# Kernel tuning notes

Hardware: AMD Instinct MI355X
Metric: run time of the kernel (lower is better)

The kernel has to match this reference:

```python
import jax, jax.numpy as jnp
import numpy as np

SIGMA_PRIOR = 0.5   # sigma init kwarg; logvar_prior = log(sigma), sigma_prior = exp(logvar_prior) = sigma
TEMP = 1.0
LN_EPS = 1e-5
DIM, NQ, NK = 256, 512, 512


def setup_inputs() -> dict:
    key = jax.random.key(0)
    ks = jax.random.split(key, 10)
    s = 1.0 / np.sqrt(DIM)
    return {
        "Q": jax.random.normal(ks[0], (NQ, DIM), jnp.float32),
        "K": jax.random.normal(ks[1], (NK, DIM), jnp.float32),
        "V": jax.random.normal(ks[2], (NK, DIM), jnp.float32),
        "eps": jax.random.normal(ks[3], (NQ, NK), jnp.float32),
        # prior MLP: Linear(dim,dim) -> ReLU -> Linear(dim,1)
        "W1p": jax.random.normal(ks[4], (DIM, DIM), jnp.float32) * s,
        "b1p": jnp.zeros((DIM,), jnp.float32),
        "w2p": jax.random.normal(ks[5], (DIM,), jnp.float32) * s,
        "b2p": jnp.zeros((), jnp.float32),
        # posterior MLP: Linear(2*dim, dim) -> ReLU
        "Wpost": jax.random.normal(ks[6], (DIM, 2 * DIM), jnp.float32) * s,
        "bpost": jnp.zeros((DIM,), jnp.float32),
        # mu / logvar heads: Linear(dim, 1)
        "w_mu": jax.random.normal(ks[7], (DIM,), jnp.float32) * s,
        "b_mu": jnp.zeros((), jnp.float32),
        "w_lv": jax.random.normal(ks[8], (DIM,), jnp.float32) * s,
        "b_lv": jnp.zeros((), jnp.float32),
        # output LayerNorm(dim)
        "gamma": jnp.ones((DIM,), jnp.float32),
        "beta": jnp.zeros((DIM,), jnp.float32),
    }


def reference(Q, K, V, eps, W1p, b1p, w2p, b2p, Wpost, bpost,
              w_mu, b_mu, w_lv, b_lv, gamma, beta):
    dim = Q.shape[-1]
    sigma_prior = jnp.float32(SIGMA_PRIOR)

    # --- prior: mlp_prior(K) per key; broadcast over queries (identical math to K_exp) ---
    h = jax.nn.relu(K @ W1p.T + b1p)                       # [Nk, dim]
    mu_prior = h @ w2p + b2p - 0.5 * sigma_prior ** 2      # [Nk]

    # --- posterior: Linear on cat([Q_exp, K_exp]) == Q@Wq^T + K@Wk^T + b ---
    Wq, Wk = Wpost[:, :dim], Wpost[:, dim:]
    latent = jax.nn.relu((Q @ Wq.T)[:, None, :] + (K @ Wk.T + bpost)[None, :, :])  # [Nq, Nk, dim]
    phi = latent @ w_mu + b_mu                             # [Nq, Nk]
    logvar = latent @ w_lv + b_lv                          # [Nq, Nk]
    sig = jnp.exp(0.5 * logvar)
    mu = phi - 0.5 * sig ** 2

    # --- KL(prior || posterior form used by the module) ---
    term0 = jnp.log(sigma_prior / sig)
    term1 = (sig ** 2 + (mu - mu_prior[None, :]) ** 2) / (2.0 * sigma_prior ** 2)
    kl = jnp.mean(term0 + term1 - 0.5)

    # --- reparameterized sample, softmax weights, context ---
    samples = jnp.exp(mu + sig * eps) / TEMP               # [Nq, Nk]
    weights = jax.nn.softmax(samples, axis=-1)
    context = weights @ V                                  # [Nq, dim]

    # --- LayerNorm(dim) ---
    m = jnp.mean(context, axis=-1, keepdims=True)
    v = jnp.var(context, axis=-1, keepdims=True)
    out = (context - m) / jnp.sqrt(v + LN_EPS) * gamma + beta
    return (out, kl)
```

## Files before the change

kernel.cpp:

```cpp
#include <hip/hip_runtime.h>
#include <math.h>

#define DIM 256
#define NQ  512
#define NK  512

#define WS_A   0
#define WS_B   (NQ*DIM)
#define WS_MP  (WS_B + NK*DIM)
#define WS_S   (WS_MP + 512)
#define WS_P   (WS_S + NQ*NK)

__global__ __launch_bounds__(512) void k1_precompute(
    const float* __restrict__ Q, const float* __restrict__ Km,
    const float* __restrict__ W1p, const float* __restrict__ b1p,
    const float* __restrict__ w2p, const float* __restrict__ b2p,
    const float* __restrict__ Wpost, const float* __restrict__ bpost,
    float* __restrict__ A, float* __restrict__ B, float* __restrict__ mu_prior)
{
    __shared__ float X_lds[4][DIM];
    __shared__ float red[2][4][260];
    const int tid = threadIdx.x;
    const int bid = blockIdx.x;

    const int job = bid >> 7;
    const int r0  = (bid & 127) * 4;
    const float* X = (job == 0) ? Q : Km;
    const float* W = (job == 2) ? W1p : Wpost;
    const int wstride = (job == 2) ? DIM : 2 * DIM;
    const int wcol    = (job == 1) ? DIM : 0;

    if (tid < 256) {
        int row = tid >> 6, c4 = tid & 63;
        *(float4*)&X_lds[row][c4 * 4] = *(const float4*)&X[(r0 + row) * DIM + c4 * 4];
    }
    __syncthreads();

    const int c  = tid & 255;
    const int dh = tid >> 8;
    const float* wrow = W + c * wstride + wcol + dh * 128;
    const float* xrow0 = &X_lds[0][dh * 128];

    float acc0 = 0.f, acc1 = 0.f, acc2 = 0.f, acc3 = 0.f;
    #pragma unroll 8
    for (int d0 = 0; d0 < 128; d0 += 4) {
        float4 w4 = *(const float4*)&wrow[d0];
        float4 x0 = *(const float4*)&xrow0[d0];
        float4 x1 = *(const float4*)&xrow0[DIM + d0];
        float4 x2 = *(const float4*)&xrow0[2 * DIM + d0];
        float4 x3 = *(const float4*)&xrow0[3 * DIM + d0];
        acc0 = fmaf(x0.x, w4.x, acc0); acc0 = fmaf(x0.y, w4.y, acc0);
        acc0 = fmaf(x0.z, w4.z, acc0); acc0 = fmaf(x0.w, w4.w, acc0);
        acc1 = fmaf(x1.x, w4.x, acc1); acc1 = fmaf(x1.y, w4.y, acc1);
        acc1 = fmaf(x1.z, w4.z, acc1); acc1 = fmaf(x1.w, w4.w, acc1);
        acc2 = fmaf(x2.x, w4.x, acc2); acc2 = fmaf(x2.y, w4.y, acc2);
        acc2 = fmaf(x2.z, w4.z, acc2); acc2 = fmaf(x2.w, w4.w, acc2);
        acc3 = fmaf(x3.x, w4.x, acc3); acc3 = fmaf(x3.y, w4.y, acc3);
        acc3 = fmaf(x3.z, w4.z, acc3); acc3 = fmaf(x3.w, w4.w, acc3);
    }
    red[dh][0][c] = acc0; red[dh][1][c] = acc1;
    red[dh][2][c] = acc2; red[dh][3][c] = acc3;
    __syncthreads();

    if (job < 2) {
        if (tid < 256) {
            #pragma unroll
            for (int r = 0; r < 4; ++r) {
                float v = red[0][r][c] + red[1][r][c];
                if (job == 0) A[(r0 + r) * DIM + c] = v;
                else          B[(r0 + r) * DIM + c] = v + bpost[c];
            }
        }
    } else {
        if (tid < 256) {
            float b1 = b1p[c], w2 = w2p[c];
            #pragma unroll
            for (int r = 0; r < 4; ++r)
                red[0][r][c] = fmaxf(red[0][r][c] + red[1][r][c] + b1, 0.f) * w2;
        }
        __syncthreads();
        int w = tid >> 6, lane = tid & 63;
        if (w < 4) {
            float v = red[0][w][lane] + red[0][w][lane + 64]
                    + red[0][w][lane + 128] + red[0][w][lane + 192];
            #pragma unroll
            for (int off = 32; off; off >>= 1) v += __shfl_xor(v, off);
            if (lane == 0) mu_prior[r0 + w] = v + b2p[0] - 0.125f;
        }
    }
}

__global__ __launch_bounds__(512) void k2_latent(
    const float* __restrict__ A, const float* __restrict__ B,
    const float* __restrict__ mu_prior, const float* __restrict__ eps,
    const float* __restrict__ w_mu, const float* __restrict__ b_mu,
    const float* __restrict__ w_lv, const float* __restrict__ b_lv,
    float* __restrict__ samples, float* __restrict__ partials)
{
    __shared__ float A_lds[32][260];
    __shared__ float B_lds[32][260];
    __shared__ float wm[DIM], wl[DIM];
    __shared__ float red[2][256][9];
    __shared__ float wred[8];
    const int tid = threadIdx.x;
    const int bq0 = (blockIdx.x >> 4) * 32;
    const int bk0 = (blockIdx.x & 15) * 32;

    #pragma unroll
    for (int i = 0; i < 4; ++i) {
        int f4 = tid + 512 * i;
        int row = f4 >> 6, c4 = f4 & 63;
        *(float4*)&A_lds[row][c4 * 4] = *(const float4*)&A[(bq0 + row) * DIM + c4 * 4];
        *(float4*)&B_lds[row][c4 * 4] = *(const float4*)&B[(bk0 + row) * DIM + c4 * 4];
    }
    if (tid < 256) { wm[tid] = w_mu[tid]; wl[tid] = w_lv[tid]; }
    __syncthreads();

    const int l  = tid & 255;
    const int dh = tid >> 8;
    const int tq = l >> 4, tk = l & 15;
    const int db = dh * 128;

    float p00 = 0, p01 = 0, p10 = 0, p11 = 0;
    float l00 = 0, l01 = 0, l10 = 0, l11 = 0;

    #pragma unroll 4
    for (int dd = 0; dd < 128; dd += 4) {
        int d0 = db + dd;
        float4 a0 = *(const float4*)&A_lds[tq][d0];
        float4 a1 = *(const float4*)&A_lds[tq + 16][d0];
        float4 b0 = *(const float4*)&B_lds[tk][d0];
        float4 b1 = *(const float4*)&B_lds[tk + 16][d0];
        float4 m4 = *(const float4*)&wm[d0];
        float4 v4 = *(const float4*)&wl[d0];
#define STEP(c) { float r_;                                                      \
        r_ = fmaxf(a0.c + b0.c, 0.f); p00 = fmaf(r_, m4.c, p00); l00 = fmaf(r_, v4.c, l00); \
        r_ = fmaxf(a0.c + b1.c, 0.f); p01 = fmaf(r_, m4.c, p01); l01 = fmaf(r_, v4.c, l01); \
        r_ = fmaxf(a1.c + b0.c, 0.f); p10 = fmaf(r_, m4.c, p10); l10 = fmaf(r_, v4.c, l10); \
        r_ = fmaxf(a1.c + b1.c, 0.f); p11 = fmaf(r_, m4.c, p11); l11 = fmaf(r_, v4.c, l11); }
        STEP(x) STEP(y) STEP(z) STEP(w)
#undef STEP
    }

    red[dh][l][0] = p00; red[dh][l][1] = l00;
    red[dh][l][2] = p01; red[dh][l][3] = l01;
    red[dh][l][4] = p10; red[dh][l][5] = l10;
    red[dh][l][6] = p11; red[dh][l][7] = l11;
    __syncthreads();

    float kls = 0.f;
    if (tid < 256) {
        const float bmu = b_mu[0], blv = b_lv[0];
        const int qa = bq0 + tq, qb = qa + 16;
        const int ka = bk0 + tk, kb = ka + 16;
        const float mpa = mu_prior[ka], mpb = mu_prior[kb];
        const float C0 = -0.69314718056f - 0.5f;

#define FINISH(i, q, k, mp) {                                        \
        float pacc = red[0][tid][2*(i)]   + red[1][tid][2*(i)];      \
        float lacc = red[0][tid][2*(i)+1] + red[1][tid][2*(i)+1];    \
        float lv   = lacc + blv;                                     \
        float phi  = pacc + bmu;                                     \
        float sig  = __expf(0.5f * lv);                              \
        float sig2 = sig * sig;                                      \
        float mu   = phi - 0.5f * sig2;                              \
        float dm   = mu - (mp);                                      \
        kls += C0 - 0.5f * lv + 2.f * (sig2 + dm * dm);              \
        samples[(q) * NK + (k)] = __expf(mu + sig * eps[(q) * NK + (k)]); }

        FINISH(0, qa, ka, mpa)
        FINISH(1, qa, kb, mpb)
        FINISH(2, qb, ka, mpa)
        FINISH(3, qb, kb, mpb)
#undef FINISH
    }

    #pragma unroll
    for (int off = 32; off; off >>= 1) kls += __shfl_xor(kls, off);
    if ((tid & 63) == 0) wred[tid >> 6] = kls;
    __syncthreads();
    if (tid == 0) {
        float s = 0.f;
        #pragma unroll
        for (int i = 0; i < 8; ++i) s += wred[i];
        partials[blockIdx.x] = s;
    }
}

__global__ __launch_bounds__(512) void k3_output(
    const float* __restrict__ samples, const float* __restrict__ V,
    const float* __restrict__ gamma, const float* __restrict__ beta,
    const float* __restrict__ partials, float* __restrict__ out)
{
    __shared__ float w_lds[2][NK];
    __shared__ float redbuf[16][DIM];
    __shared__ float sred[8], sred2[8], klr[8], sinv[2];
    const int tid = threadIdx.x;
    const int q0 = blockIdx.x * 2;

    if (blockIdx.x == 0) {
        float v = (tid < 256) ? partials[tid] : 0.f;
        #pragma unroll
        for (int off = 32; off; off >>= 1) v += __shfl_xor(v, off);
        if ((tid & 63) == 0) klr[tid >> 6] = v;
        __syncthreads();
        if (tid == 0) {
            float s = 0.f;
            #pragma unroll
            for (int i = 0; i < 8; ++i) s += klr[i];
            out[NQ * DIM] = s * (1.f / (float)(NQ * NK));
        }
    }

    #pragma unroll
    for (int r = 0; r < 2; ++r) {
        float sv = samples[(q0 + r) * NK + tid];
        float m = sv;
        #pragma unroll
        for (int off = 32; off; off >>= 1) m = fmaxf(m, __shfl_xor(m, off));
        if ((tid & 63) == 0) sred[tid >> 6] = m;
        __syncthreads();
        m = fmaxf(fmaxf(fmaxf(sred[0], sred[1]), fmaxf(sred[2], sred[3])),
                  fmaxf(fmaxf(sred[4], sred[5]), fmaxf(sred[6], sred[7])));
        float e = __expf(sv - m);
        w_lds[r][tid] = e;
        float sum = e;
        #pragma unroll
        for (int off = 32; off; off >>= 1) sum += __shfl_xor(sum, off);
        __syncthreads();
        if ((tid & 63) == 0) sred[tid >> 6] = sum;
        __syncthreads();
        if (tid == 0) {
            float s = 0.f;
            #pragma unroll
            for (int i = 0; i < 8; ++i) s += sred[i];
            sinv[r] = 1.f / s;
        }
        __syncthreads();
    }

    const int g = tid & 63, s = tid >> 6;
    float a00 = 0, a01 = 0, a02 = 0, a03 = 0;
    float a10 = 0, a11 = 0, a12 = 0, a13 = 0;
    const float* vp = V + s * 64 * DIM + 4 * g;
    #pragma unroll 8
    for (int i = 0; i < 64; ++i) {
        float4 v4 = *(const float4*)(vp + i * DIM);
        int k = s * 64 + i;
        float w0 = w_lds[0][k], w1 = w_lds[1][k];
        a00 = fmaf(w0, v4.x, a00); a01 = fmaf(w0, v4.y, a01);
        a02 = fmaf(w0, v4.z, a02); a03 = fmaf(w0, v4.w, a03);
        a10 = fmaf(w1, v4.x, a10); a11 = fmaf(w1, v4.y, a11);
        a12 = fmaf(w1, v4.z, a12); a13 = fmaf(w1, v4.w, a13);
    }
    *(float4*)&redbuf[s * 2 + 0][4 * g] = make_float4(a00, a01, a02, a03);
    *(float4*)&redbuf[s * 2 + 1][4 * g] = make_float4(a10, a11, a12, a13);
    __syncthreads();

    const int r = tid >> 8, col = tid & 255;
    float c = 0.f;
    #pragma unroll
    for (int j = 0; j < 8; ++j) c += redbuf[j * 2 + r][col];
    c *= sinv[r];
    float s1v = c, s2v = c * c;
    #pragma unroll
    for (int off = 32; off; off >>= 1) {
        s1v += __shfl_xor(s1v, off);
        s2v += __shfl_xor(s2v, off);
    }
    if ((tid & 63) == 0) { sred[tid >> 6] = s1v; sred2[tid >> 6] = s2v; }
    __syncthreads();
    float mean = (sred[4 * r] + sred[4 * r + 1] + sred[4 * r + 2] + sred[4 * r + 3]) * (1.f / DIM);
    float msq  = (sred2[4 * r] + sred2[4 * r + 1] + sred2[4 * r + 2] + sred2[4 * r + 3]) * (1.f / DIM);
    float var  = msq - mean * mean;
    out[(q0 + r) * DIM + col] = (c - mean) * rsqrtf(var + 1e-5f) * gamma[col] + beta[col];
}

extern "C" void kernel_launch(void* const* d_in, const int* in_sizes, int n_in,
                              void* d_out, int out_size, void* d_ws, size_t ws_size,
                              hipStream_t stream)
{
    (void)in_sizes; (void)n_in; (void)out_size; (void)ws_size;
    const float* Q     = (const float*)d_in[0];
    const float* K     = (const float*)d_in[1];
    const float* V     = (const float*)d_in[2];
    const float* eps   = (const float*)d_in[3];
    const float* W1p   = (const float*)d_in[4];
    const float* b1p   = (const float*)d_in[5];
    const float* w2p   = (const float*)d_in[6];
    const float* b2p   = (const float*)d_in[7];
    const float* Wpost = (const float*)d_in[8];
    const float* bpost = (const float*)d_in[9];
    const float* w_mu  = (const float*)d_in[10];
    const float* b_mu  = (const float*)d_in[11];
    const float* w_lv  = (const float*)d_in[12];
    const float* b_lv  = (const float*)d_in[13];
    const float* gamma = (const float*)d_in[14];
    const float* beta  = (const float*)d_in[15];
    float* out = (float*)d_out;
    float* wsf = (float*)d_ws;

    float* A        = wsf + WS_A;
    float* B        = wsf + WS_B;
    float* mu_prior = wsf + WS_MP;
    float* samples  = wsf + WS_S;
    float* partials = wsf + WS_P;

    k1_precompute<<<dim3(384), dim3(512), 0, stream>>>(
        Q, K, W1p, b1p, w2p, b2p, Wpost, bpost, A, B, mu_prior);
    k2_latent<<<dim3(256), dim3(512), 0, stream>>>(
        A, B, mu_prior, eps, w_mu, b_mu, w_lv, b_lv, samples, partials);
    k3_output<<<dim3(256), dim3(512), 0, stream>>>(
        samples, V, gamma, beta, partials, out);
}
```

Before: 123.2 us.

## Fuse three kernels into one cooperative kernel with grid-wide syncs

Replaces the three separate launches (precompute, latent, output) with a single cooperative kernel of 256 blocks that uses grid.sync() between phases and a union of shared-memory layouts. To fit the phase-1 work into 256 blocks, the Q/K projection blocks now process 8 rows each instead of 4. The aim is to remove the launch gaps and inter-kernel drain between stages. In exchange it adds grid-barrier cost, and the first phase has fewer, heavier blocks.

Result: slower. 196.9 us (+59.8%).

```diff
diff --git a/kernel.cpp b/kernel.cpp
--- a/kernel.cpp
+++ b/kernel.cpp
@@ -1,5 +1,8 @@
 #include <hip/hip_runtime.h>
+#include <hip/hip_cooperative_groups.h>
 #include <math.h>
+
+namespace cg = cooperative_groups;
 
 #define DIM 256
 #define NQ  512
@@ -11,269 +14,293 @@
 #define WS_S   (WS_MP + 512)
 #define WS_P   (WS_S + NQ*NK)
 
-__global__ __launch_bounds__(512) void k1_precompute(
+struct P1 {
+    float X[8][DIM];
+    float red[2][8][260];
+};
+struct P2 {
+    float A[32][260];
+    float B[32][260];
+    float wm[DIM], wl[DIM];
+    float red[2][256][9];
+    float wred[8];
+};
+struct P3 {
+    float w[2][NK];
+    float redbuf[16][DIM];
+    float sred[8], sred2[8], klr[8], sinv[2];
+};
+union SmemU { P1 p1; P2 p2; P3 p3; };
+
+__global__ __launch_bounds__(512) void fused_kernel(
     const float* __restrict__ Q, const float* __restrict__ Km,
+    const float* __restrict__ V, const float* __restrict__ eps,
     const float* __restrict__ W1p, const float* __restrict__ b1p,
     const float* __restrict__ w2p, const float* __restrict__ b2p,
     const float* __restrict__ Wpost, const float* __restrict__ bpost,
-    float* __restrict__ A, float* __restrict__ B, float* __restrict__ mu_prior)
-{
-    __shared__ float X_lds[4][DIM];
-    __shared__ float red[2][4][260];
-    const int tid = threadIdx.x;
-    const int bid = blockIdx.x;
-
-    const int job = bid >> 7;
-    const int r0  = (bid & 127) * 4;
-    const float* X = (job == 0) ? Q : Km;
-    const float* W = (job == 2) ? W1p : Wpost;
-    const int wstride = (job == 2) ? DIM : 2 * DIM;
-    const int wcol    = (job == 1) ? DIM : 0;
-
-    if (tid < 256) {
-        int row = tid >> 6, c4 = tid & 63;
-        *(float4*)&X_lds[row][c4 * 4] = *(const float4*)&X[(r0 + row) * DIM + c4 * 4];
-    }
-    __syncthreads();
-
-    const int c  = tid & 255;
-    const int dh = tid >> 8;
-    const float* wrow = W + c * wstride + wcol + dh * 128;
-    const float* xrow0 = &X_lds[0][dh * 128];
-
-    float acc0 = 0.f, acc1 = 0.f, acc2 = 0.f, acc3 = 0.f;
-    #pragma unroll 8
-    for (int d0 = 0; d0 < 128; d0 += 4) {
-        float4 w4 = *(const float4*)&wrow[d0];
-        float4 x0 = *(const float4*)&xrow0[d0];
-        float4 x1 = *(const float4*)&xrow0[DIM + d0];
-        float4 x2 = *(const float4*)&xrow0[2 * DIM + d0];
-        float4 x3 = *(const float4*)&xrow0[3 * DIM + d0];
-        acc0 = fmaf(x0.x, w4.x, acc0); acc0 = fmaf(x0.y, w4.y, acc0);
-        acc0 = fmaf(x0.z, w4.z, acc0); acc0 = fmaf(x0.w, w4.w, acc0);
-        acc1 = fmaf(x1.x, w4.x, acc1); acc1 = fmaf(x1.y, w4.y, acc1);
-        acc1 = fmaf(x1.z, w4.z, acc1); acc1 = fmaf(x1.w, w4.w, acc1);
-        acc2 = fmaf(x2.x, w4.x, acc2); acc2 = fmaf(x2.y, w4.y, acc2);
-        acc2 = fmaf(x2.z, w4.z, acc2); acc2 = fmaf(x2.w, w4.w, acc2);
-        acc3 = fmaf(x3.x, w4.x, acc3); acc3 = fmaf(x3.y, w4.y, acc3);
-        acc3 = fmaf(x3.z, w4.z, acc3); acc3 = fmaf(x3.w, w4.w, acc3);
-    }
-    red[dh][0][c] = acc0; red[dh][1][c] = acc1;
-    red[dh][2][c] = acc2; red[dh][3][c] = acc3;
-    __syncthreads();
-
-    if (job < 2) {
-        if (tid < 256) {
-            #pragma unroll
-            for (int r = 0; r < 4; ++r) {
-                float v = red[0][r][c] + red[1][r][c];
-                if (job == 0) A[(r0 + r) * DIM + c] = v;
-                else          B[(r0 + r) * DIM + c] = v + bpost[c];
-            }
-        }
-    } else {
-        if (tid < 256) {
-            float b1 = b1p[c], w2 = w2p[c];
-            #pragma unroll
-            for (int r = 0; r < 4; ++r)
-                red[0][r][c] = fmaxf(red[0][r][c] + red[1][r][c] + b1, 0.f) * w2;
-        }
-        __syncthreads();
-        int w = tid >> 6, lane = tid & 63;
-        if (w < 4) {
-            float v = red[0][w][lane] + red[0][w][lane + 64]
-                    + red[0][w][lane + 128] + red[0][w][lane + 192];
-            #pragma unroll
-            for (int off = 32; off; off >>= 1) v += __shfl_xor(v, off);
-            if (lane == 0) mu_prior[r0 + w] = v + b2p[0] - 0.125f;
-        }
-    }
-}
-
-__global__ __launch_bounds__(512) void k2_latent(
-    const float* __restrict__ A, const float* __restrict__ B,
-    const float* __restrict__ mu_prior, const float* __restrict__ eps,
     const float* __restrict__ w_mu, const float* __restrict__ b_mu,
     const float* __restrict__ w_lv, const float* __restrict__ b_lv,
-    float* __restrict__ samples, float* __restrict__ partials)
+    const float* __restrict__ gamma, const float* __restrict__ beta,
+    float* __restrict__ out,
+    float* __restrict__ Ag, float* __restrict__ Bg, float* __restrict__ MPg,
+    float* __restrict__ Sg, float* __restrict__ Pg)
 {
-    __shared__ float A_lds[32][260];
-    __shared__ float B_lds[32][260];
-    __shared__ float wm[DIM], wl[DIM];
-    __shared__ float red[2][256][9];
-    __shared__ float wred[8];
+    __shared__ SmemU sm;
+    cg::grid_group grid = cg::this_grid();
     const int tid = threadIdx.x;
-    const int bq0 = (blockIdx.x >> 4) * 32;
-    const int bk0 = (blockIdx.x & 15) * 32;
-
-    #pragma unroll
-    for (int i = 0; i < 4; ++i) {
-        int f4 = tid + 512 * i;
-        int row = f4 >> 6, c4 = f4 & 63;
-        *(float4*)&A_lds[row][c4 * 4] = *(const float4*)&A[(bq0 + row) * DIM + c4 * 4];
-        *(float4*)&B_lds[row][c4 * 4] = *(const float4*)&B[(bk0 + row) * DIM + c4 * 4];
+    const int b   = blockIdx.x;
+
+    {
+        const int job = (b < 64) ? 0 : (b < 128) ? 1 : 2;
+        const float* X = (job == 0) ? Q : Km;
+        const int r0    = (job < 2) ? ((b & 63) * 8) : ((b - 128) * 4);
+        const int nrows = (job < 2) ? 8 : 4;
+
+        for (int i = tid; i < nrows * 64; i += 512) {
+            int row = i >> 6, c4 = i & 63;
+            *(float4*)&sm.p1.X[row][c4 * 4] = *(const float4*)&X[(r0 + row) * DIM + c4 * 4];
+        }
+        __syncthreads();
+
+        const int c = tid & 255, dh = tid >> 8;
+        const float* W = (job == 2) ? W1p : Wpost;
+        const int wstride = (job == 2) ? DIM : 2 * DIM;
+        const int wcol    = (job == 1) ? DIM : 0;
+        const float* wrow = W + c * wstride + wcol + dh * 128;
+        const float* xb = &sm.p1.X[0][dh * 128];
+
+        if (job < 2) {
+            float acc[8] = {0.f, 0.f, 0.f, 0.f, 0.f, 0.f, 0.f, 0.f};
+            #pragma unroll 8
+            for (int d0 = 0; d0 < 128; d0 += 4) {
+                float4 w4 = *(const float4*)&wrow[d0];
+                #pragma unroll
+                for (int r = 0; r < 8; ++r) {
+                    float4 x4 = *(const float4*)&xb[r * DIM + d0];
+                    acc[r] = fmaf(x4.x, w4.x, acc[r]);
+                    acc[r] = fmaf(x4.y, w4.y, acc[r]);
+                    acc[r] = fmaf(x4.z, w4.z, acc[r]);
+                    acc[r] = fmaf(x4.w, w4.w, acc[r]);
+                }
+            }
+            #pragma unroll
+            for (int r = 0; r < 8; ++r) sm.p1.red[dh][r][c] = acc[r];
+            __syncthreads();
+            if (tid < 256) {
+                if (job == 0) {
+                    #pragma unroll
+                    for (int r = 0; r < 8; ++r)
+                        Ag[(r0 + r) * DIM + c] = sm.p1.red[0][r][c] + sm.p1.red[1][r][c];
+                } else {
+                    float bp = bpost[c];
+                    #pragma unroll
+                    for (int r = 0; r < 8; ++r)
+                        Bg[(r0 + r) * DIM + c] = sm.p1.red[0][r][c] + sm.p1.red[1][r][c] + bp;
+                }
+            }
+        } else {
+            float acc[4] = {0.f, 0.f, 0.f, 0.f};
+            #pragma unroll 8
+            for (int d0 = 0; d0 < 128; d0 += 4) {
+                float4 w4 = *(const float4*)&wrow[d0];
+                #pragma unroll
+                for (int r = 0; r < 4; ++r) {
+                    float4 x4 = *(const float4*)&xb[r * DIM + d0];
+                    acc[r] = fmaf(x4.x, w4.x, acc[r]);
+                    acc[r] = fmaf(x4.y, w4.y, acc[r]);
+                    acc[r] = fmaf(x4.z, w4.z, acc[r]);
+                    acc[r] = fmaf(x4.w, w4.w, acc[r]);
+                }
+            }
+            #pragma unroll
+            for (int r = 0; r < 4; ++r) sm.p1.red[dh][r][c] = acc[r];
+            __syncthreads();
+            if (tid < 256) {
+                float b1 = b1p[c], w2 = w2p[c];
+                #pragma unroll
+                for (int r = 0; r < 4; ++r)
+                    sm.p1.red[0][r][c] =
+                        fmaxf(sm.p1.red[0][r][c] + sm.p1.red[1][r][c] + b1, 0.f) * w2;
+            }
+            __syncthreads();
+            const int w = tid >> 6, lane = tid & 63;
+            if (w < 4) {
+                float v = sm.p1.red[0][w][lane] + sm.p1.red[0][w][lane + 64]
+                        + sm.p1.red[0][w][lane + 128] + sm.p1.red[0][w][lane + 192];
+                #pragma unroll
+                for (int off = 32; off; off >>= 1) v += __shfl_xor(v, off);
+                if (lane == 0) MPg[r0 + w] = v + b2p[0] - 0.125f;
+            }
+        }
     }
-    if (tid < 256) { wm[tid] = w_mu[tid]; wl[tid] = w_lv[tid]; }
-    __syncthreads();
-
-    const int l  = tid & 255;
-    const int dh = tid >> 8;
-    const int tq = l >> 4, tk = l & 15;
-    const int db = dh * 128;
-
-    float p00 = 0, p01 = 0, p10 = 0, p11 = 0;
-    float l00 = 0, l01 = 0, l10 = 0, l11 = 0;
-
-    #pragma unroll 4
-    for (int dd = 0; dd < 128; dd += 4) {
-        int d0 = db + dd;
-        float4 a0 = *(const float4*)&A_lds[tq][d0];
-        float4 a1 = *(const float4*)&A_lds[tq + 16][d0];
-        float4 b0 = *(const float4*)&B_lds[tk][d0];
-        float4 b1 = *(const float4*)&B_lds[tk + 16][d0];
-        float4 m4 = *(const float4*)&wm[d0];
-        float4 v4 = *(const float4*)&wl[d0];
+    grid.sync();
+
+    {
+        const int bq0 = (b >> 4) * 32;
+        const int bk0 = (b & 15) * 32;
+
+        #pragma unroll
+        for (int i = 0; i < 4; ++i) {
+            int f4 = tid + 512 * i;
+            int row = f4 >> 6, c4 = f4 & 63;
+            *(float4*)&sm.p2.A[row][c4 * 4] = *(const float4*)&Ag[(bq0 + row) * DIM + c4 * 4];
+            *(float4*)&sm.p2.B[row][c4 * 4] = *(const float4*)&Bg[(bk0 + row) * DIM + c4 * 4];
+        }
+        if (tid < 256) { sm.p2.wm[tid] = w_mu[tid]; sm.p2.wl[tid] = w_lv[tid]; }
+        __syncthreads();
+
+        const int l  = tid & 255;
+        const int dh = tid >> 8;
+        const int tq = l >> 4, tk = l & 15;
+        const int db = dh * 128;
+
+        float p00 = 0, p01 = 0, p10 = 0, p11 = 0;
+        float l00 = 0, l01 = 0, l10 = 0, l11 = 0;
+
+        #pragma unroll 4
+        for (int dd = 0; dd < 128; dd += 4) {
+            int d0 = db + dd;
+            float4 a0 = *(const float4*)&sm.p2.A[tq][d0];
+            float4 a1 = *(const float4*)&sm.p2.A[tq + 16][d0];
+            float4 b0 = *(const float4*)&sm.p2.B[tk][d0];
+            float4 b1 = *(const float4*)&sm.p2.B[tk + 16][d0];
+            float4 m4 = *(const float4*)&sm.p2.wm[d0];
+            float4 v4 = *(const float4*)&sm.p2.wl[d0];
 #define STEP(c) { float r_;                                                      \
-        r_ = fmaxf(a0.c + b0.c, 0.f); p00 = fmaf(r_, m4.c, p00); l00 = fmaf(r_, v4.c, l00); \
-        r_ = fmaxf(a0.c + b1.c, 0.f); p01 = fmaf(r_, m4.c, p01); l01 = fmaf(r_, v4.c, l01); \
-        r_ = fmaxf(a1.c + b0.c, 0.f); p10 = fmaf(r_, m4.c, p10); l10 = fmaf(r_, v4.c, l10); \
-        r_ = fmaxf(a1.c + b1.c, 0.f); p11 = fmaf(r_, m4.c, p11); l11 = fmaf(r_, v4.c, l11); }
-        STEP(x) STEP(y) STEP(z) STEP(w)
+            r_ = fmaxf(a0.c + b0.c, 0.f); p00 = fmaf(r_, m4.c, p00); l00 = fmaf(r_, v4.c, l00); \
+            r_ = fmaxf(a0.c + b1.c, 0.f); p01 = fmaf(r_, m4.c, p01); l01 = fmaf(r_, v4.c, l01); \
+            r_ = fmaxf(a1.c + b0.c, 0.f); p10 = fmaf(r_, m4.c, p10); l10 = fmaf(r_, v4.c, l10); \
+            r_ = fmaxf(a1.c + b1.c, 0.f); p11 = fmaf(r_, m4.c, p11); l11 = fmaf(r_, v4.c, l11); }
+            STEP(x) STEP(y) STEP(z) STEP(w)
 #undef STEP
-    }
-
-    red[dh][l][0] = p00; red[dh][l][1] = l00;
-    red[dh][l][2] = p01; red[dh][l][3] = l01;
-    red[dh][l][4] = p10; red[dh][l][5] = l10;
-    red[dh][l][6] = p11; red[dh][l][7] = l11;
-    __syncthreads();
-
-    float kls = 0.f;
-    if (tid < 256) {
-        const float bmu = b_mu[0], blv = b_lv[0];
-        const int qa = bq0 + tq, qb = qa + 16;
-        const int ka = bk0 + tk, kb = ka + 16;
-        const float mpa = mu_prior[ka], mpb = mu_prior[kb];
-        const float C0 = -0.69314718056f - 0.5f;
-
-#define FINISH(i, q, k, mp) {                                        \
-        float pacc = red[0][tid][2*(i)]   + red[1][tid][2*(i)];      \
-        float lacc = red[0][tid][2*(i)+1] + red[1][tid][2*(i)+1];    \
-        float lv   = lacc + blv;                                     \
-        float phi  = pacc + bmu;                                     \
-        float sig  = __expf(0.5f * lv);                              \
-        float sig2 = sig * sig;                                      \
-        float mu   = phi - 0.5f * sig2;                              \
-        float dm   = mu - (mp);                                      \
-        kls += C0 - 0.5f * lv + 2.f * (sig2 + dm * dm);              \
-        samples[(q) * NK + (k)] = __expf(mu + sig * eps[(q) * NK + (k)]); }
-
-        FINISH(0, qa, ka, mpa)
-        FINISH(1, qa, kb, mpb)
-        FINISH(2, qb, ka, mpa)
-        FINISH(3, qb, kb, mpb)
+        }
+
+        sm.p2.red[dh][l][0] = p00; sm.p2.red[dh][l][1] = l00;
+        sm.p2.red[dh][l][2] = p01; sm.p2.red[dh][l][3] = l01;
+        sm.p2.red[dh][l][4] = p10; sm.p2.red[dh][l][5] = l10;
+        sm.p2.red[dh][l][6] = p11; sm.p2.red[dh][l][7] = l11;
+        __syncthreads();
+
+        float kls = 0.f;
+        if (tid < 256) {
+            const float bmu = b_mu[0], blv = b_lv[0];
+            const int qa = bq0 + tq, qb = qa + 16;
+            const int ka = bk0 + tk, kb = ka + 16;
+            const float mpa = MPg[ka], mpb = MPg[kb];
+            const float C0 = -0.69314718056f - 0.5f;
+
+#define FINISH(i, q, k, mp) {                                            \
+            float pacc = sm.p2.red[0][tid][2*(i)]   + sm.p2.red[1][tid][2*(i)];   \
+            float lacc = sm.p2.red[0][tid][2*(i)+1] + sm.p2.red[1][tid][2*(i)+1]; \
+            float lv   = lacc + blv;                                     \
+            float phi  = pacc + bmu;                                     \
+            float sig  = __expf(0.5f * lv);                              \
+            float sig2 = sig * sig;                                      \
+            float mu   = phi - 0.5f * sig2;                              \
+            float dm   = mu - (mp);                                      \
+            kls += C0 - 0.5f * lv + 2.f * (sig2 + dm * dm);              \
+            Sg[(q) * NK + (k)] = __expf(mu + sig * eps[(q) * NK + (k)]); }
+
+            FINISH(0, qa, ka, mpa)
+            FINISH(1, qa, kb, mpb)
+            FINISH(2, qb, ka, mpa)
+            FINISH(3, qb, kb, mpb)
 #undef FINISH
-    }
-
-    #pragma unroll
-    for (int off = 32; off; off >>= 1) kls += __shfl_xor(kls, off);
-    if ((tid & 63) == 0) wred[tid >> 6] = kls;
-    __syncthreads();
-    if (tid == 0) {
-        float s = 0.f;
-        #pragma unroll
-        for (int i = 0; i < 8; ++i) s += wred[i];
-        partials[blockIdx.x] = s;
-    }
-}
-
-__global__ __launch_bounds__(512) void k3_output(
-    const float* __restrict__ samples, const float* __restrict__ V,
-    const float* __restrict__ gamma, const float* __restrict__ beta,
-    const float* __restrict__ partials, float* __restrict__ out)
-{
-    __shared__ float w_lds[2][NK];
-    __shared__ float redbuf[16][DIM];
-    __shared__ float sred[8], sred2[8], klr[8], sinv[2];
-    const int tid = threadIdx.x;
-    const int q0 = blockIdx.x * 2;
-
-    if (blockIdx.x == 0) {
-        float v = (tid < 256) ? partials[tid] : 0.f;
-        #pragma unroll
-        for (int off = 32; off; off >>= 1) v += __shfl_xor(v, off);
-        if ((tid & 63) == 0) klr[tid >> 6] = v;
+        }
+
+        #pragma unroll
+        for (int off = 32; off; off >>= 1) kls += __shfl_xor(kls, off);
+        if ((tid & 63) == 0) sm.p2.wred[tid >> 6] = kls;
         __syncthreads();
         if (tid == 0) {
             float s = 0.f;
             #pragma unroll
-            for (int i = 0; i < 8; ++i) s += klr[i];
-            out[NQ * DIM] = s * (1.f / (float)(NQ * NK));
+            for (int i = 0; i < 8; ++i) s += sm.p2.wred[i];
+            Pg[b] = s;
         }
     }
-
-    #pragma unroll
-    for (int r = 0; r < 2; ++r) {
-        float sv = samples[(q0 + r) * NK + tid];
-        float m = sv;
-        #pragma unroll
-        for (int off = 32; off; off >>= 1) m = fmaxf(m, __shfl_xor(m, off));
-        if ((tid & 63) == 0) sred[tid >> 6] = m;
-        __syncthreads();
-        m = fmaxf(fmaxf(fmaxf(sred[0], sred[1]), fmaxf(sred[2], sred[3])),
-                  fmaxf(fmaxf(sred[4], sred[5]), fmaxf(sred[6], sred[7])));
-        float e = __expf(sv - m);
-        w_lds[r][tid] = e;
-        float sum = e;
-        #pragma unroll
-        for (int off = 32; off; off >>= 1) sum += __shfl_xor(sum, off);
-        __syncthreads();
-        if ((tid & 63) == 0) sred[tid >> 6] = sum;
-        __syncthreads();
-        if (tid == 0) {
-            float s = 0.f;
-            #pragma unroll
-            for (int i = 0; i < 8; ++i) s += sred[i];
-            sinv[r] = 1.f / s;
-        }
-        __syncthreads();
+    grid.sync();
+
+    {
+        const int q0 = b * 2;
+
+        if (b == 0) {
+            float v = (tid < 256) ? Pg[tid] : 0.f;
+            #pragma unroll
+            for (int off = 32; off; off >>= 1) v += __shfl_xor(v, off);
+            if ((tid & 63) == 0) sm.p3.klr[tid >> 6] = v;
+            __syncthreads();
+            if (tid == 0) {
+                float s = 0.f;
+                #pragma unroll
+                for (int i = 0; i < 8; ++i) s += sm.p3.klr[i];
+                out[NQ * DIM] = s * (1.f / (float)(NQ * NK));
+            }
+        }
+
+        #pragma unroll
+        for (int r = 0; r < 2; ++r) {
+            float sv = Sg[(q0 + r) * NK + tid];
+            float m = sv;
+            #pragma unroll
+            for (int off = 32; off; off >>= 1) m = fmaxf(m, __shfl_xor(m, off));
+            if ((tid & 63) == 0) sm.p3.sred[tid >> 6] = m;
+            __syncthreads();
+            m = fmaxf(fmaxf(fmaxf(sm.p3.sred[0], sm.p3.sred[1]), fmaxf(sm.p3.sred[2], sm.p3.sred[3])),
+                      fmaxf(fmaxf(sm.p3.sred[4], sm.p3.sred[5]), fmaxf(sm.p3.sred[6], sm.p3.sred[7])));
+            float e = __expf(sv - m);
+            sm.p3.w[r][tid] = e;
+            float sum = e;
+            #pragma unroll
+            for (int off = 32; off; off >>= 1) sum += __shfl_xor(sum, off);
+            __syncthreads();
+            if ((tid & 63) == 0) sm.p3.sred[tid >> 6] = sum;
+            __syncthreads();
+            if (tid == 0) {
+                float s = 0.f;
+                #pragma unroll
+                for (int i = 0; i < 8; ++i) s += sm.p3.sred[i];
+                sm.p3.sinv[r] = 1.f / s;
+            }
+            __syncthreads();
+        }
+
+        const int g = tid & 63, s = tid >> 6;
+        float a00 = 0, a01 = 0, a02 = 0, a03 = 0;
+        float a10 = 0, a11 = 0, a12 = 0, a13 = 0;
+        const float* vp = V + s * 64 * DIM + 4 * g;
+        #pragma unroll 8
+        for (int i = 0; i < 64; ++i) {
+            float4 v4 = *(const float4*)(vp + i * DIM);
+            int k = s * 64 + i;
+            float w0 = sm.p3.w[0][k], w1 = sm.p3.w[1][k];
+            a00 = fmaf(w0, v4.x, a00); a01 = fmaf(w0, v4.y, a01);
+            a02 = fmaf(w0, v4.z, a02); a03 = fmaf(w0, v4.w, a03);
+            a10 = fmaf(w1, v4.x, a10); a11 = fmaf(w1, v4.y, a11);
+            a12 = fmaf(w1, v4.z, a12); a13 = fmaf(w1, v4.w, a13);
+        }
+        *(float4*)&sm.p3.redbuf[s * 2 + 0][4 * g] = make_float4(a00, a01, a02, a03);
+        *(float4*)&sm.p3.redbuf[s * 2 + 1][4 * g] = make_float4(a10, a11, a12, a13);
+        __syncthreads();
+
+        const int r = tid >> 8, col = tid & 255;
+        float c = 0.f;
+        #pragma unroll
+        for (int j = 0; j < 8; ++j) c += sm.p3.redbuf[j * 2 + r][col];
+        c *= sm.p3.sinv[r];
+        float s1v = c, s2v = c * c;
+        #pragma unroll
+        for (int off = 32; off; off >>= 1) {
+            s1v += __shfl_xor(s1v, off);
+            s2v += __shfl_xor(s2v, off);
+        }
+        if ((tid & 63) == 0) { sm.p3.sred[tid >> 6] = s1v; sm.p3.sred2[tid >> 6] = s2v; }
+        __syncthreads();
+        float mean = (sm.p3.sred[4 * r] + sm.p3.sred[4 * r + 1] + sm.p3.sred[4 * r + 2] + sm.p3.sred[4 * r + 3]) * (1.f / DIM);
+        float msq  = (sm.p3.sred2[4 * r] + sm.p3.sred2[4 * r + 1] + sm.p3.sred2[4 * r + 2] + sm.p3.sred2[4 * r + 3]) * (1.f / DIM);
+        float var  = msq - mean * mean;
+        out[(q0 + r) * DIM + col] = (c - mean) * rsqrtf(var + 1e-5f) * gamma[col] + beta[col];
     }
-
-    const int g = tid & 63, s = tid >> 6;
-    float a00 = 0, a01 = 0, a02 = 0, a03 = 0;
-    float a10 = 0, a11 = 0, a12 = 0, a13 = 0;
-    const float* vp = V + s * 64 * DIM + 4 * g;
-    #pragma unroll 8
-    for (int i = 0; i < 64; ++i) {
-        float4 v4 = *(const float4*)(vp + i * DIM);
-        int k = s * 64 + i;
-        float w0 = w_lds[0][k], w1 = w_lds[1][k];
-        a00 = fmaf(w0, v4.x, a00); a01 = fmaf(w0, v4.y, a01);
-        a02 = fmaf(w0, v4.z, a02); a03 = fmaf(w0, v4.w, a03);
-        a10 = fmaf(w1, v4.x, a10); a11 = fmaf(w1, v4.y, a11);
-        a12 = fmaf(w1, v4.z, a12); a13 = fmaf(w1, v4.w, a13);
-    }
-    *(float4*)&redbuf[s * 2 + 0][4 * g] = make_float4(a00, a01, a02, a03);
-    *(float4*)&redbuf[s * 2 + 1][4 * g] = make_float4(a10, a11, a12, a13);
-    __syncthreads();
-
-    const int r = tid >> 8, col = tid & 255;
-    float c = 0.f;
-    #pragma unroll
-    for (int j = 0; j < 8; ++j) c += redbuf[j * 2 + r][col];
-    c *= sinv[r];
-    float s1v = c, s2v = c * c;
-    #pragma unroll
-    for (int off = 32; off; off >>= 1) {
-        s1v += __shfl_xor(s1v, off);
-        s2v += __shfl_xor(s2v, off);
-    }
-    if ((tid & 63) == 0) { sred[tid >> 6] = s1v; sred2[tid >> 6] = s2v; }
-    __syncthreads();
-    float mean = (sred[4 * r] + sred[4 * r + 1] + sred[4 * r + 2] + sred[4 * r + 3]) * (1.f / DIM);
-    float msq  = (sred2[4 * r] + sred2[4 * r + 1] + sred2[4 * r + 2] + sred2[4 * r + 3]) * (1.f / DIM);
-    float var  = msq - mean * mean;
-    out[(q0 + r) * DIM + col] = (c - mean) * rsqrtf(var + 1e-5f) * gamma[col] + beta[col];
 }
 
 extern "C" void kernel_launch(void* const* d_in, const int* in_sizes, int n_in,
@@ -282,7 +309,7 @@
 {
     (void)in_sizes; (void)n_in; (void)out_size; (void)ws_size;
     const float* Q     = (const float*)d_in[0];
-    const float* K     = (const float*)d_in[1];
+    const float* Km    = (const float*)d_in[1];
     const float* V     = (const float*)d_in[2];
     const float* eps   = (const float*)d_in[3];
     const float* W1p   = (const float*)d_in[4];
@@ -300,16 +327,19 @@
     float* out = (float*)d_out;
     float* wsf = (float*)d_ws;
 
-    float* A        = wsf + WS_A;
-    float* B        = wsf + WS_B;
-    float* mu_prior = wsf + WS_MP;
-    float* samples  = wsf + WS_S;
-    float* partials = wsf + WS_P;
-
-    k1_precompute<<<dim3(384), dim3(512), 0, stream>>>(
-        Q, K, W1p, b1p, w2p, b2p, Wpost, bpost, A, B, mu_prior);
-    k2_latent<<<dim3(256), dim3(512), 0, stream>>>(
-        A, B, mu_prior, eps, w_mu, b_mu, w_lv, b_lv, samples, partials);
-    k3_output<<<dim3(256), dim3(512), 0, stream>>>(
-        samples, V, gamma, beta, partials, out);
+    float* Ag  = wsf + WS_A;
+    float* Bg  = wsf + WS_B;
+    float* MPg = wsf + WS_MP;
+    float* Sg  = wsf + WS_S;
+    float* Pg  = wsf + WS_P;
+
+    void* args[] = {
+        (void*)&Q, (void*)&Km, (void*)&V, (void*)&eps,
+        (void*)&W1p, (void*)&b1p, (void*)&w2p, (void*)&b2p,
+        (void*)&Wpost, (void*)&bpost, (void*)&w_mu, (void*)&b_mu,
+        (void*)&w_lv, (void*)&b_lv, (void*)&gamma, (void*)&beta,
+        (void*)&out, (void*)&Ag, (void*)&Bg, (void*)&MPg, (void*)&Sg, (void*)&Pg
+    };
+    hipLaunchCooperativeKernel((void*)fused_kernel, dim3(256), dim3(512),
+                               args, 0, stream);
 }
```
